# Kernel tuning notes

Measured on AMD Instinct MI355X. Metric: run time of the kernel, lower is better.

Reference implementation:

```python
import jax, jax.numpy as jnp
import numpy as np

B, MAX_OBJS, D = 8, 12, 512
NUM_OBJ, NUM_ACT, NUM_TRS = 37, 6, 3
EMBED = 128
NUM_AA = 100
NUM_CLASSES = 300
ACT_THRES = 0.5
K = MAX_OBJS * NUM_ACT            # 72 candidate (object, action) slots
FINAL_DIM = 2 * (D + 2 * EMBED)   # 1536
# All ordered pairs (i, j), i != j, in lexicographic order. itertools.permutations
# over a sorted index subset is exactly the valid-masked subsequence of this list.
_pairs = np.array([(i, j) for i in range(K) for j in range(K) if i != j], dtype=np.int64)
PAIR_I = jnp.asarray(_pairs[:, 0])
PAIR_J = jnp.asarray(_pairs[:, 1])
P = _pairs.shape[0]               # K*(K-1) = 5112 (static max num pairs)


def setup_inputs() -> dict:
    key = jax.random.key(0)
    ks = jax.random.split(key, 12)
    inp = jax.random.normal(ks[0], (B, MAX_OBJS, D), jnp.float32)
    objmask = jnp.ones((B, MAX_OBJS), jnp.float32)
    # -1 marks 'no composite-action target' for that (obj, act) slot
    AAidxs_tgts = jax.random.randint(ks[1], (B, K), -1, NUM_AA)
    TR_tgts = jax.random.uniform(ks[2], (B, K, K, NUM_TRS), jnp.float32)
    obj_act_lookup = jax.random.randint(ks[3], (NUM_OBJ, NUM_ACT), 0, NUM_AA)
    aa_aa_tr_lookup = jax.random.randint(ks[4], (NUM_AA, NUM_AA, NUM_TRS), 0, NUM_CLASSES)
    s = lambda k, shape: (jax.random.normal(k, shape, jnp.float32) * 0.02)
    return {
        'inp': inp, 'objmask': objmask,
        'TR_tgts': TR_tgts,
        'W_obj': s(ks[5], (NUM_OBJ, D)), 'b_obj': jnp.zeros((NUM_OBJ,), jnp.float32),
        'W_act': s(ks[6], (NUM_ACT, D)), 'b_act': jnp.zeros((NUM_ACT,), jnp.float32),
        'W_tr': s(ks[7], (NUM_TRS, FINAL_DIM)), 'b_tr': jnp.zeros((NUM_TRS,), jnp.float32),
        'W_ne': s(ks[8], (NUM_CLASSES, D)), 'b_ne': jnp.zeros((NUM_CLASSES,), jnp.float32),
        'obj_emb': s(ks[9], (NUM_OBJ, EMBED)), 'act_emb': s(ks[10], (NUM_ACT, EMBED)),
        'AAidxs_tgts': AAidxs_tgts,
        'obj_act_lookup': obj_act_lookup,
        'aa_aa_tr_lookup': aa_aa_tr_lookup,
    }


def reference(inp, objmask, TR_tgts, W_obj, b_obj, W_act, b_act, W_tr, b_tr,
              W_ne, b_ne, obj_emb, act_emb, AAidxs_tgts, obj_act_lookup,
              aa_aa_tr_lookup):
    # training branch (is_eval=False); obj_act_lookup only used in eval branch
    exp_objmask = jnp.repeat(objmask, NUM_ACT, axis=1)                # [B,K]
    masked = inp * objmask[:, :, None]
    pooled = masked.sum(axis=1) / objmask.sum(axis=1, keepdims=True)  # [B,D]
    non_exist_out = pooled @ W_ne.T + b_ne                            # [B,C]
    obj_out = inp @ W_obj.T + b_obj                                   # [B,MO,NO]
    act_out = inp @ W_act.T + b_act                                   # [B,MO,NA]

    posb_action_idxs = jnp.tile(jnp.arange(NUM_ACT), (B, MAX_OBJS))   # [B,K]
    pred_obj_idxs = jnp.repeat(jnp.argmax(obj_out, axis=-1), NUM_ACT, axis=1)  # [B,K]
    posb_inputs = jnp.repeat(inp, NUM_ACT, axis=1)                    # [B,K,D]

    pred_act = (jax.nn.sigmoid(act_out.reshape(B, K)) > ACT_THRES).astype(jnp.float32)
    pred_act = pred_act * exp_objmask
    selected = (pred_act == 1.0) & (AAidxs_tgts != -1)                # [B,K]
    aaidx = jnp.where(selected, AAidxs_tgts, -1)

    posb_obj_emb = obj_emb[pred_obj_idxs]                             # [B,K,E]
    posb_act_emb = act_emb[posb_action_idxs]                          # [B,K,E]
    comp = jnp.concatenate([posb_inputs, posb_obj_emb, posb_act_emb], axis=-1)  # [B,K,FINAL/2]

    # pack valid pairs to the front (stable sort preserves lexicographic order,
    # matching itertools.permutations over the sorted selected index set)
    valid = selected[:, PAIR_I] & selected[:, PAIR_J]                 # [B,P]
    order = jnp.argsort(~valid, axis=1, stable=True)                  # [B,P]
    valid_p = jnp.take_along_axis(valid, order, axis=1)
    i_p = jnp.take_along_axis(jnp.broadcast_to(PAIR_I, (B, P)), order, axis=1)
    j_p = jnp.take_along_axis(jnp.broadcast_to(PAIR_J, (B, P)), order, axis=1)
    b_ix = jnp.arange(B)[:, None]

    pair_out = jnp.where(valid_p[..., None],
                         jnp.concatenate([comp[b_ix, i_p], comp[b_ix, j_p]], axis=-1),
                         -1.0)                                        # [B,P,FINAL_DIM]
    pair_logits = pair_out @ W_tr.T + b_tr                            # [B,P,3]

    aai = aaidx[b_ix, i_p]
    aaj = aaidx[b_ix, j_p]
    ca = aa_aa_tr_lookup[jnp.maximum(aai, 0), jnp.maximum(aaj, 0)]    # [B,P,3]
    ca = jnp.where(valid_p[..., None], ca, -1)
    tr_targets = jnp.where(valid_p[..., None], TR_tgts[b_ix, i_p, j_p], -1.0)

    # diag(logit) @ one_hot(ca) then masked max over pairs == segment max per class
    flat_logit = pair_logits.reshape(B, P * NUM_TRS)
    flat_ca = ca.reshape(B, P * NUM_TRS)
    flat_valid = jnp.repeat(valid_p, NUM_TRS, axis=1)
    seg = jnp.where(flat_valid, flat_ca, NUM_CLASSES)                 # dump invalid to extra segment
    seg_max = jax.vmap(lambda l, s: jax.ops.segment_max(l, s, num_segments=NUM_CLASSES + 1))(
        flat_logit, seg)[:, :NUM_CLASSES]                             # [B,C]
    counts = jax.vmap(lambda s: jax.ops.segment_sum(jnp.ones_like(s), s, num_segments=NUM_CLASSES + 1))(
        seg)[:, :NUM_CLASSES]
    exist = counts > 0
    final_outputs = jnp.where(exist, seg_max, non_exist_out)          # [B,C]

    return final_outputs, pair_logits, tr_targets, act_out, obj_out
```

## Files before the change

### kernel.cpp

```cpp
#include <hip/hip_runtime.h>
#include <hip/hip_bf16.h>

#define Bn    8
#define MO    12
#define Dd    512
#define NOBJ  37
#define NACT  6
#define NTRS  3
#define EMB   128
#define NAA   100
#define NCLS  300
#define Kk    72
#define Pp    5112
#define HALF  768
#define FD    1536

#define OUT_FINAL 0
#define OUT_PLOG  (Bn*NCLS)
#define OUT_TTGT  (OUT_PLOG + Bn*Pp*NTRS)
#define OUT_ACT   (OUT_TTGT + Bn*Pp*NTRS)
#define OUT_OBJ   (OUT_ACT + Bn*Kk)

#define WS_LINP 0
#define WS_EO   (WS_LINP + Bn*MO*6)
#define WS_EA   (WS_EO + NOBJ*6)
#define WS_INV  (WS_EA + NACT*6)
#define WS_NE   840
#define WS_OBJ  (WS_NE + Bn*NCLS)
#define WS_ACT  (WS_OBJ + Bn*MO*NOBJ)
#define WS_SEG  (WS_ACT + Bn*Kk)
#define WS_CNT  (WS_SEG + Bn*NCLS)
#define NZERO   (Bn*NCLS + Bn)

__device__ __forceinline__ unsigned fmap(float f) {
  unsigned u = __float_as_uint(f);
  return (u & 0x80000000u) ? ~u : (u | 0x80000000u);
}
__device__ __forceinline__ float funmap(unsigned u) {
  return __uint_as_float((u & 0x80000000u) ? (u & 0x7fffffffu) : ~u);
}

__device__ __forceinline__ float wreduce(float v) {
#pragma unroll
  for (int off = 32; off > 0; off >>= 1) v += __shfl_xor(v, off, 64);
  return v;
}

__device__ __forceinline__ float dotW(const float* __restrict__ wrow,
                                      float4 x0, float4 x1, int lane) {
  const float4* w4 = (const float4*)wrow;
  float4 w0 = w4[lane], w1 = w4[lane + 64];
  float s0 = fmaf(w0.x, x0.x, fmaf(w0.y, x0.y, fmaf(w0.z, x0.z, w0.w * x0.w)));
  float s1 = fmaf(w1.x, x1.x, fmaf(w1.y, x1.y, fmaf(w1.z, x1.z, w1.w * x1.w)));
  return wreduce(s0 + s1);
}

__device__ __forceinline__ float dot512_wave(const float* __restrict__ a,
                                             const float* __restrict__ b, int lane) {
  const float4* b4 = (const float4*)b;
  return dotW(a, b4[lane], b4[lane + 64], lane);
}

__device__ __forceinline__ float dot128_wave(const float* __restrict__ a,
                                             const float* __restrict__ b, int lane) {
  const float2* a2 = (const float2*)a;
  const float2* b2 = (const float2*)b;
  float2 x = a2[lane], y = b2[lane];
  return wreduce(fmaf(x.x, y.x, x.y * y.y));
}

#define W_OBJ_E  (Bn*MO*NOBJ)
#define W_ACT_E  (W_OBJ_E + Bn*Kk)
#define W_LINP_E (W_ACT_E + Bn*MO*6)
#define W_EO_E   (W_LINP_E + NOBJ*6)
#define W_EA_E   (W_EO_E + NACT*6)
#define W_INV_E  (W_EA_E + NTRS)
#define W_NE_E   (W_INV_E + Bn*NCLS)
#define W_TOT    (W_NE_E + 38)

__global__ __launch_bounds__(256) void k1(
    const float* __restrict__ inp, const float* __restrict__ objmask,
    const float* __restrict__ W_obj, const float* __restrict__ b_obj,
    const float* __restrict__ W_act, const float* __restrict__ b_act,
    const float* __restrict__ W_tr, const float* __restrict__ b_tr,
    const float* __restrict__ W_ne, const float* __restrict__ b_ne,
    const float* __restrict__ obj_emb, const float* __restrict__ act_emb,
    float* __restrict__ out, float* __restrict__ ws)
{
  int gt = blockIdx.x * 256 + threadIdx.x;
  int w = gt >> 6, lane = gt & 63;

  if (w < W_OBJ_E) {
    int b = w / (MO*NOBJ), r = w % (MO*NOBJ), o = r / NOBJ, c = r % NOBJ;
    float v = dot512_wave(W_obj + c*Dd, inp + (b*MO + o)*Dd, lane) + b_obj[c];
    if (!lane) { out[OUT_OBJ + (b*MO + o)*NOBJ + c] = v; ws[WS_OBJ + (b*MO + o)*NOBJ + c] = v; }
  } else if (w < W_ACT_E) {
    int r = w - W_OBJ_E, b = r / Kk, k = r % Kk, o = k / NACT, a = k % NACT;
    float v = dot512_wave(W_act + a*Dd, inp + (b*MO + o)*Dd, lane) + b_act[a];
    if (!lane) { out[OUT_ACT + b*Kk + k] = v; ws[WS_ACT + b*Kk + k] = v; }
  } else if (w < W_LINP_E) {
    int r = w - W_ACT_E, b = r / (MO*6), r2 = r % (MO*6), o = r2 / 6, th = r2 % 6;
    int t = th >> 1, h = th & 1;
    float v = dot512_wave(W_tr + t*FD + h*HALF, inp + (b*MO + o)*Dd, lane);
    if (!lane) ws[WS_LINP + (b*MO + o)*6 + th] = v;
  } else if (w < W_EO_E) {
    int r = w - W_LINP_E, oc = r / 6, th = r % 6, t = th >> 1, h = th & 1;
    float v = dot128_wave(W_tr + t*FD + h*HALF + Dd, obj_emb + oc*EMB, lane);
    if (!lane) ws[WS_EO + oc*6 + th] = v;
  } else if (w < W_INV_E) {
    if (w < W_EA_E) {
      int r = w - W_EO_E, a = r / 6, th = r % 6, t = th >> 1, h = th & 1;
      float v = dot128_wave(W_tr + t*FD + h*HALF + Dd + EMB, act_emb + a*EMB, lane);
      if (!lane) ws[WS_EA + a*6 + th] = v;
    } else {
      int t = w - W_EA_E;
      const float4* w4 = (const float4*)(W_tr + t*FD);
      float s = 0.f;
#pragma unroll
      for (int i = 0; i < 6; ++i) { float4 x = w4[lane + 64*i]; s += x.x + x.y + x.z + x.w; }
      s = wreduce(s);
      if (!lane) ws[WS_INV + t] = b_tr[t] - s;
    }
  } else if (w < W_NE_E) {
    int r = w - W_INV_E, b = r / NCLS, c = r % NCLS;
    const float4* i4 = (const float4*)inp;
    float msum = 0.f;
    float4 p0 = make_float4(0.f, 0.f, 0.f, 0.f), p1 = p0;
#pragma unroll
    for (int o = 0; o < MO; ++o) {
      float m = objmask[b*MO + o];
      msum += m;
      float4 v0 = i4[(b*MO + o)*128 + lane];
      float4 v1 = i4[(b*MO + o)*128 + lane + 64];
      p0.x = fmaf(m, v0.x, p0.x); p0.y = fmaf(m, v0.y, p0.y);
      p0.z = fmaf(m, v0.z, p0.z); p0.w = fmaf(m, v0.w, p0.w);
      p1.x = fmaf(m, v1.x, p1.x); p1.y = fmaf(m, v1.y, p1.y);
      p1.z = fmaf(m, v1.z, p1.z); p1.w = fmaf(m, v1.w, p1.w);
    }
    float v = dotW(W_ne + c*Dd, p0, p1, lane) / msum + b_ne[c];
    if (!lane) ws[WS_NE + b*NCLS + c] = v;
  } else if (w < W_TOT) {
    int idx = (w - W_NE_E)*64 + lane;
    if (idx < NZERO) ((unsigned*)ws)[WS_SEG + idx] = 0u;
  }
}

#define NSLICE 20

__global__ __launch_bounds__(256) void k2(
    const float* __restrict__ objmask, const float* __restrict__ TRt,
    const float* __restrict__ b_tr, const int* __restrict__ AA,
    const int* __restrict__ aalut,
    float* __restrict__ out, float* __restrict__ ws)
{
  __shared__ float s_L[Kk*6];
  __shared__ float s_inv[NTRS];
  __shared__ int s_sel[Kk], s_aa[Kk], s_C[Kk], s_pred[MO], s_T, s_last;

  int b = blockIdx.x / NSLICE, slice = blockIdx.x % NSLICE;
  int tid = threadIdx.x;

  if (tid < MO) {
    const float* p = ws + WS_OBJ + (b*MO + tid)*NOBJ;
    float best = p[0]; int bi = 0;
    for (int c = 1; c < NOBJ; ++c) { float v = p[c]; if (v > best) { best = v; bi = c; } }
    s_pred[tid] = bi;
  } else if (tid < MO + NTRS) {
    s_inv[tid - MO] = ws[WS_INV + (tid - MO)];
  } else if (tid >= 64 && tid < 64 + Kk) {
    int k = tid - 64, o = k / NACT;
    int aa = AA[b*Kk + k];
    int sel = (ws[WS_ACT + b*Kk + k] > 0.f) && (objmask[b*MO + o] == 1.0f) && (aa != -1);
    s_sel[k] = sel;
    s_aa[k] = sel ? aa : -1;
  }
  __syncthreads();
  for (int m = tid; m < Kk*6; m += 256) {
    int k = m / 6, th = m % 6, t = th >> 1, h = th & 1;
    int o = k / NACT, a = k % NACT;
    float v = ws[WS_LINP + (b*MO + o)*6 + th] + ws[WS_EO + s_pred[o]*6 + th]
            + ws[WS_EA + a*6 + th];
    if (h == 0) v += b_tr[t];
    s_L[m] = v;
  }
  if (tid == 0) {
    int c = 0;
    for (int k = 0; k < Kk; ++k) { s_C[k] = c; c += s_sel[k]; }
    s_T = c;
  }
  __syncthreads();

  int T = s_T, Vtot = T*(T-1);
  int q = slice*256 + tid;
  if (q < Pp) {
    float* plog = out + OUT_PLOG + (size_t)b*Pp*NTRS;
    float* ttgt = out + OUT_TTGT + (size_t)b*Pp*NTRS;
    int i = q / (Kk-1);
    int jj = q - i*(Kk-1);
    int j = jj + (jj >= i ? 1 : 0);
    int si = s_sel[i], sj = s_sel[j];
    int vb = s_C[i]*(T-1) + (si ? (s_C[j] - (i < j ? 1 : 0)) : 0);
    bool valid = si && sj;
    int pos = valid ? vb : (Vtot + q - vb);
    float l0, l1, l2;
    if (valid) {
      l0 = s_L[i*6+0] + s_L[j*6+1];
      l1 = s_L[i*6+2] + s_L[j*6+3];
      l2 = s_L[i*6+4] + s_L[j*6+5];
    } else { l0 = s_inv[0]; l1 = s_inv[1]; l2 = s_inv[2]; }
    int ob = pos*3;
    plog[ob+0] = l0; plog[ob+1] = l1; plog[ob+2] = l2;
    if (valid) {
      const float* tr = TRt + (((size_t)b*Kk + i)*Kk + j)*NTRS;
      ttgt[ob+0] = tr[0]; ttgt[ob+1] = tr[1]; ttgt[ob+2] = tr[2];
      int base = (s_aa[i]*NAA + s_aa[j])*NTRS;
      unsigned* seg = (unsigned*)ws + WS_SEG + b*NCLS;
      atomicMax(&seg[aalut[base+0]], fmap(l0));
      atomicMax(&seg[aalut[base+1]], fmap(l1));
      atomicMax(&seg[aalut[base+2]], fmap(l2));
    } else {
      ttgt[ob+0] = -1.f; ttgt[ob+1] = -1.f; ttgt[ob+2] = -1.f;
    }
  }

  __threadfence();
  __syncthreads();
  if (tid == 0) {
    unsigned old = atomicAdd((unsigned*)ws + WS_CNT + b, 1u);
    s_last = (old == NSLICE - 1);
  }
  __syncthreads();
  if (s_last) {
    __threadfence();
    for (int c = tid; c < NCLS; c += 256) {
      unsigned u = atomicMax((unsigned*)ws + WS_SEG + b*NCLS + c, 0u);
      out[OUT_FINAL + b*NCLS + c] = u ? funmap(u) : ws[WS_NE + b*NCLS + c];
    }
  }
}

extern "C" void kernel_launch(void* const* d_in, const int* in_sizes, int n_in,
                              void* d_out, int out_size, void* d_ws, size_t ws_size,
                              hipStream_t stream) {
  (void)in_sizes; (void)n_in; (void)ws_size; (void)out_size;
  const float* inp      = (const float*)d_in[0];
  const float* objmask  = (const float*)d_in[1];
  const float* TRt      = (const float*)d_in[2];
  const float* W_obj    = (const float*)d_in[3];
  const float* b_obj    = (const float*)d_in[4];
  const float* W_act    = (const float*)d_in[5];
  const float* b_act    = (const float*)d_in[6];
  const float* W_tr     = (const float*)d_in[7];
  const float* b_tr     = (const float*)d_in[8];
  const float* W_ne     = (const float*)d_in[9];
  const float* b_ne     = (const float*)d_in[10];
  const float* obj_emb  = (const float*)d_in[11];
  const float* act_emb  = (const float*)d_in[12];
  const int*   AA       = (const int*)d_in[13];
  const int*   aalut    = (const int*)d_in[15];
  float* out = (float*)d_out;
  float* ws  = (float*)d_ws;

  hipLaunchKernelGGL(k1, dim3((W_TOT + 3) / 4), dim3(256), 0, stream,
                     inp, objmask, W_obj, b_obj, W_act, b_act, W_tr, b_tr,
                     W_ne, b_ne, obj_emb, act_emb, out, ws);
  hipLaunchKernelGGL(k2, dim3(Bn * NSLICE), dim3(256), 0, stream,
                     objmask, TRt, b_tr, AA, aalut, out, ws);
}
```

Baseline: 109.7 us.

## Use one block per batch with shared-memory segment max, dropping global atomics

k2 previously used 20 slice blocks per batch, each doing global atomicMax into a workspace segment array. A global counter then let the last block finalize the outputs, and k1 zeroed that workspace. Now one block per batch loops over all pairs, accumulates the segment max in shared memory, and writes the final outputs directly. This removes the global atomics, the zeroing, the threadfences and the last-block handshake, but cuts k2 parallelism from 160 blocks to 8.

```diff
diff --git a/kernel.cpp b/kernel.cpp
--- a/kernel.cpp
+++ b/kernel.cpp
@@ -28,9 +28,6 @@
 #define WS_NE   840
 #define WS_OBJ  (WS_NE + Bn*NCLS)
 #define WS_ACT  (WS_OBJ + Bn*MO*NOBJ)
-#define WS_SEG  (WS_ACT + Bn*Kk)
-#define WS_CNT  (WS_SEG + Bn*NCLS)
-#define NZERO   (Bn*NCLS + Bn)
 
 __device__ __forceinline__ unsigned fmap(float f) {
   unsigned u = __float_as_uint(f);
@@ -75,8 +72,7 @@
 #define W_EO_E   (W_LINP_E + NOBJ*6)
 #define W_EA_E   (W_EO_E + NACT*6)
 #define W_INV_E  (W_EA_E + NTRS)
-#define W_NE_E   (W_INV_E + Bn*NCLS)
-#define W_TOT    (W_NE_E + 38)
+#define W_TOT    (W_INV_E + Bn*NCLS)
 
 __global__ __launch_bounds__(256) void k1(
     const float* __restrict__ inp, const float* __restrict__ objmask,
@@ -121,7 +117,7 @@
       s = wreduce(s);
       if (!lane) ws[WS_INV + t] = b_tr[t] - s;
     }
-  } else if (w < W_NE_E) {
+  } else if (w < W_TOT) {
     int r = w - W_INV_E, b = r / NCLS, c = r % NCLS;
     const float4* i4 = (const float4*)inp;
     float msum = 0.f;
@@ -139,13 +135,8 @@
     }
     float v = dotW(W_ne + c*Dd, p0, p1, lane) / msum + b_ne[c];
     if (!lane) ws[WS_NE + b*NCLS + c] = v;
-  } else if (w < W_TOT) {
-    int idx = (w - W_NE_E)*64 + lane;
-    if (idx < NZERO) ((unsigned*)ws)[WS_SEG + idx] = 0u;
-  }
-}
-
-#define NSLICE 20
+  }
+}
 
 __global__ __launch_bounds__(256) void k2(
     const float* __restrict__ objmask, const float* __restrict__ TRt,
@@ -155,25 +146,28 @@
 {
   __shared__ float s_L[Kk*6];
   __shared__ float s_inv[NTRS];
-  __shared__ int s_sel[Kk], s_aa[Kk], s_C[Kk], s_pred[MO], s_T, s_last;
-
-  int b = blockIdx.x / NSLICE, slice = blockIdx.x % NSLICE;
+  __shared__ unsigned s_seg[NCLS];
+  __shared__ int s_sel[Kk], s_aa[Kk], s_C[Kk], s_pred[MO], s_T;
+
+  int b = blockIdx.x;
   int tid = threadIdx.x;
 
   if (tid < MO) {
     const float* p = ws + WS_OBJ + (b*MO + tid)*NOBJ;
     float best = p[0]; int bi = 0;
+#pragma unroll
     for (int c = 1; c < NOBJ; ++c) { float v = p[c]; if (v > best) { best = v; bi = c; } }
     s_pred[tid] = bi;
-  } else if (tid < MO + NTRS) {
-    s_inv[tid - MO] = ws[WS_INV + (tid - MO)];
   } else if (tid >= 64 && tid < 64 + Kk) {
     int k = tid - 64, o = k / NACT;
     int aa = AA[b*Kk + k];
     int sel = (ws[WS_ACT + b*Kk + k] > 0.f) && (objmask[b*MO + o] == 1.0f) && (aa != -1);
     s_sel[k] = sel;
     s_aa[k] = sel ? aa : -1;
-  }
+  } else if (tid >= 192 && tid < 192 + NTRS) {
+    s_inv[tid - 192] = ws[WS_INV + (tid - 192)];
+  }
+  for (int c = tid; c < NCLS; c += 256) s_seg[c] = 0u;
   __syncthreads();
   for (int m = tid; m < Kk*6; m += 256) {
     int k = m / 6, th = m % 6, t = th >> 1, h = th & 1;
@@ -191,10 +185,9 @@
   __syncthreads();
 
   int T = s_T, Vtot = T*(T-1);
-  int q = slice*256 + tid;
-  if (q < Pp) {
-    float* plog = out + OUT_PLOG + (size_t)b*Pp*NTRS;
-    float* ttgt = out + OUT_TTGT + (size_t)b*Pp*NTRS;
+  float* plog = out + OUT_PLOG + (size_t)b*Pp*NTRS;
+  float* ttgt = out + OUT_TTGT + (size_t)b*Pp*NTRS;
+  for (int q = tid; q < Pp; q += 256) {
     int i = q / (Kk-1);
     int jj = q - i*(Kk-1);
     int j = jj + (jj >= i ? 1 : 0);
@@ -214,28 +207,18 @@
       const float* tr = TRt + (((size_t)b*Kk + i)*Kk + j)*NTRS;
       ttgt[ob+0] = tr[0]; ttgt[ob+1] = tr[1]; ttgt[ob+2] = tr[2];
       int base = (s_aa[i]*NAA + s_aa[j])*NTRS;
-      unsigned* seg = (unsigned*)ws + WS_SEG + b*NCLS;
-      atomicMax(&seg[aalut[base+0]], fmap(l0));
-      atomicMax(&seg[aalut[base+1]], fmap(l1));
-      atomicMax(&seg[aalut[base+2]], fmap(l2));
+      atomicMax(&s_seg[aalut[base+0]], fmap(l0));
+      atomicMax(&s_seg[aalut[base+1]], fmap(l1));
+      atomicMax(&s_seg[aalut[base+2]], fmap(l2));
     } else {
       ttgt[ob+0] = -1.f; ttgt[ob+1] = -1.f; ttgt[ob+2] = -1.f;
     }
   }
-
-  __threadfence();
   __syncthreads();
-  if (tid == 0) {
-    unsigned old = atomicAdd((unsigned*)ws + WS_CNT + b, 1u);
-    s_last = (old == NSLICE - 1);
-  }
-  __syncthreads();
-  if (s_last) {
-    __threadfence();
-    for (int c = tid; c < NCLS; c += 256) {
-      unsigned u = atomicMax((unsigned*)ws + WS_SEG + b*NCLS + c, 0u);
-      out[OUT_FINAL + b*NCLS + c] = u ? funmap(u) : ws[WS_NE + b*NCLS + c];
-    }
+
+  for (int c = tid; c < NCLS; c += 256) {
+    unsigned u = s_seg[c];
+    out[OUT_FINAL + b*NCLS + c] = u ? funmap(u) : ws[WS_NE + b*NCLS + c];
   }
 }
 
@@ -264,6 +247,6 @@
   hipLaunchKernelGGL(k1, dim3((W_TOT + 3) / 4), dim3(256), 0, stream,
                      inp, objmask, W_obj, b_obj, W_act, b_act, W_tr, b_tr,
                      W_ne, b_ne, obj_emb, act_emb, out, ws);
-  hipLaunchKernelGGL(k2, dim3(Bn * NSLICE), dim3(256), 0, stream,
+  hipLaunchKernelGGL(k2, dim3(Bn), dim3(256), 0, stream,
                      objmask, TRt, b_tr, AA, aalut, out, ws);
 }
```

Measured after the change: 103.9 us. 5.3% less time.
